# Optimization experiments

Hardware: AMD Instinct MI355X
Metric: run time of the kernel (lower is better)

Reference implementation:

```python
import jax, jax.numpy as jnp
import numpy as np

D_MODEL = 1024
N_HEADS = 16
D_HEAD = D_MODEL // N_HEADS
BATCH = 2
SEQ = 2048


def spectral_linear(x, basis, scales):
    # (x @ U) * s @ U^T ; basis is a fixed (non-learned) square matrix
    return ((x @ basis) * scales) @ basis.T


def setup_inputs() -> dict:
    key = jax.random.key(0)
    ks = jax.random.split(key, 3)
    x = jax.random.normal(ks[0], (BATCH, SEQ, D_MODEL), dtype=jnp.float32)
    # orthonormal-ish spectral basis (random Gaussian scaled keeps values sane)
    basis = jax.random.normal(ks[1], (D_MODEL, D_MODEL), dtype=jnp.float32) / np.sqrt(D_MODEL)
    route_bias = jax.random.normal(ks[2], (N_HEADS, SEQ, SEQ), dtype=jnp.float32) * 0.02
    ones = jnp.ones((D_MODEL,), dtype=jnp.float32)
    return {
        "x": x,
        "basis": basis,
        "scale_q": ones,
        "scale_k": ones,
        "scale_v": ones,
        "scale_o": ones,
        "route_bias": route_bias,
    }


def reference(x, basis, scale_q, scale_k, scale_v, scale_o, route_bias):
    bsz, seq_len, _ = x.shape

    def split_heads(t):  # [b,s,d] -> [b,h,s,dh]
        return t.reshape(bsz, seq_len, N_HEADS, D_HEAD).transpose(0, 2, 1, 3)

    q = split_heads(spectral_linear(x, basis, scale_q))
    k = split_heads(spectral_linear(x, basis, scale_k))
    v = split_heads(spectral_linear(x, basis, scale_v))

    scores = jnp.einsum("bhqd,bhkd->bhqk", q, k) / np.sqrt(D_HEAD).astype(np.float32)
    scores = scores + route_bias[None, :, :seq_len, :seq_len]
    causal = jnp.triu(jnp.ones((seq_len, seq_len), dtype=bool), k=1)
    scores = jnp.where(causal[None, None], -jnp.inf, scores)
    attn = jax.nn.softmax(scores, axis=-1)
    out = jnp.einsum("bhqk,bhkd->bhqd", attn, v)
    out = out.transpose(0, 2, 1, 3).reshape(bsz, seq_len, D_MODEL)
    return spectral_linear(out, basis, scale_o)
```

## Files before the change

### kernel.cpp

```cpp
#include <hip/hip_runtime.h>
#include <stdint.h>

#define AS1 __attribute__((address_space(1)))
#define AS3 __attribute__((address_space(3)))

typedef __bf16 bf16x8 __attribute__((ext_vector_type(8)));
typedef float f32x4 __attribute__((ext_vector_type(4)));

#if defined(__has_builtin)
#if __has_builtin(__builtin_amdgcn_global_load_lds)
#define USE_GLL 1
#else
#define USE_GLL 0
#endif
#else
#define USE_GLL 0
#endif

static __device__ __forceinline__ unsigned short f2bf(float f) {
    union { float f; uint32_t u; } v; v.f = f;
    uint32_t u = v.u + 0x7fffu + ((v.u >> 16) & 1u);
    return (unsigned short)(u >> 16);
}

__global__ void k_f32_to_bf16(const float* __restrict__ in, unsigned short* __restrict__ out, int n) {
    int idx = (blockIdx.x * 256 + threadIdx.x) * 4;
    if (idx >= n) return;
    float4 v = *(const float4*)(in + idx);
    unsigned short r[4] = { f2bf(v.x), f2bf(v.y), f2bf(v.z), f2bf(v.w) };
    *(uint2*)(out + idx) = *(const uint2*)r;
}

__global__ void k_make_scaled(const float* __restrict__ basis,
                              const float* __restrict__ sq, const float* __restrict__ sk,
                              const float* __restrict__ sv, const float* __restrict__ so,
                              unsigned short* __restrict__ Bq, unsigned short* __restrict__ Bk,
                              unsigned short* __restrict__ Bv, unsigned short* __restrict__ Bo,
                              unsigned short* __restrict__ Ub) {
    int idx = blockIdx.x * 256 + threadIdx.x;
    int k = idx & 1023;
    float b = basis[idx];
    Bq[idx] = f2bf(b * sq[k]);
    Bk[idx] = f2bf(b * sk[k]);
    Bv[idx] = f2bf(b * sv[k]);
    Bo[idx] = f2bf(b * so[k]);
    Ub[idx] = f2bf(b);
}

__global__ void k_transpose_v(const unsigned short* __restrict__ vsb, unsigned short* __restrict__ vtb) {
    __shared__ __align__(16) unsigned short t[128 * 72];
    const int sc = blockIdx.x;
    const int bh = blockIdx.y;
    const int tid = threadIdx.x;
    #pragma unroll
    for (int rep = 0; rep < 4; ++rep) {
        int idx = rep * 256 + tid;
        int s = idx >> 3, part = idx & 7;
        *(uint4*)(t + s * 72 + part * 8) =
            *(const uint4*)(vsb + ((size_t)bh * 2048 + sc * 128 + s) * 64 + part * 8);
    }
    __syncthreads();
    #pragma unroll
    for (int rep = 0; rep < 4; ++rep) {
        int idx = rep * 256 + tid;
        int d = idx >> 4, pc = idx & 15;
        unsigned short tmp[8];
        #pragma unroll
        for (int j = 0; j < 8; ++j) tmp[j] = t[(pc * 8 + j) * 72 + d];
        *(uint4*)(vtb + ((size_t)bh * 64 + d) * 2048 + sc * 128 + pc * 8) = *(const uint4*)tmp;
    }
}

#define BK 32

__global__ __launch_bounds__(256, 2)
void k_gemm_qkv(const unsigned short* __restrict__ A,
                const unsigned short* __restrict__ B,
                unsigned short* __restrict__ qkv,
                int M, int N, int K)
{
    __shared__ __align__(16) unsigned short As[128 * BK];
    __shared__ __align__(16) unsigned short Bs[128 * BK];

    const int tid  = threadIdx.x;
    const int lane = tid & 63;
    const int w    = tid >> 6;
    const int wm   = w & 1;
    const int wn   = w >> 1;
    const int bm   = blockIdx.y;
    const int bn   = blockIdx.x;
    const int fm   = lane & 15;
    const int quad = lane >> 4;
    const int fk   = quad * 8;
    const int srow = lane >> 2;
    const int spart= lane & 3;

    f32x4 zero4 = {0.f, 0.f, 0.f, 0.f};
    f32x4 acc[4][4];
    #pragma unroll
    for (int i = 0; i < 4; ++i)
        #pragma unroll
        for (int j = 0; j < 4; ++j) acc[i][j] = zero4;

    for (int k0 = 0; k0 < K; k0 += BK) {
        #pragma unroll
        for (int t = 0; t < 2; ++t) {
            int row = w * 32 + t * 16 + srow;
            const unsigned short* ga = A + (size_t)(bm * 128 + row) * K + k0 + spart * 8;
            const unsigned short* gb = B + (size_t)(bn * 128 + row) * K + k0 + spart * 8;
#if USE_GLL
            __builtin_amdgcn_global_load_lds((const void AS1*)ga, (void AS3*)(As + w * 1024 + t * 512), 16, 0, 0);
            __builtin_amdgcn_global_load_lds((const void AS1*)gb, (void AS3*)(Bs + w * 1024 + t * 512), 16, 0, 0);
#else
            *(uint4*)(As + w * 1024 + t * 512 + lane * 8) = *(const uint4*)ga;
            *(uint4*)(Bs + w * 1024 + t * 512 + lane * 8) = *(const uint4*)gb;
#endif
        }
        __syncthreads();
        bf16x8 af[4], bfr[4];
        #pragma unroll
        for (int i = 0; i < 4; ++i) af[i] = *(const bf16x8*)(As + (wm * 64 + i * 16 + fm) * BK + fk);
        #pragma unroll
        for (int j = 0; j < 4; ++j) bfr[j] = *(const bf16x8*)(Bs + (wn * 64 + j * 16 + fm) * BK + fk);
        #pragma unroll
        for (int i = 0; i < 4; ++i)
            #pragma unroll
            for (int j = 0; j < 4; ++j)
                acc[i][j] = __builtin_amdgcn_mfma_f32_16x16x32_bf16(af[i], bfr[j], acc[i][j], 0, 0, 0);
        __syncthreads();
    }

    #pragma unroll
    for (int i = 0; i < 4; ++i)
        #pragma unroll
        for (int j = 0; j < 4; ++j)
            #pragma unroll
            for (int r = 0; r < 4; ++r) {
                int row = bm * 128 + wm * 64 + i * 16 + quad * 4 + r;
                int col = bn * 128 + wn * 64 + j * 16 + fm;
                int sec = col >> 10, cc = col & 1023;
                int bb = row >> 11, s = row & 2047;
                int hh = cc >> 6,  d = cc & 63;
                qkv[((size_t)sec << 22) + (((size_t)(bb * 16 + hh)) * 2048 + s) * 64 + d] = f2bf(acc[i][j][r]);
            }
}

template<int EPI>
__global__ __launch_bounds__(256, 2)
void k_gemm_n64(const unsigned short* __restrict__ A,
                const unsigned short* __restrict__ B,
                void* __restrict__ Cout,
                int M, int N, int K)
{
    __shared__ __align__(16) unsigned short As[128 * BK];
    __shared__ __align__(16) unsigned short Bs[64 * BK];

    const int tid  = threadIdx.x;
    const int lane = tid & 63;
    const int w    = tid >> 6;
    const int wm   = w & 1;
    const int wn   = w >> 1;
    const int bm   = blockIdx.y;
    const int bn   = blockIdx.x;
    const int fm   = lane & 15;
    const int quad = lane >> 4;
    const int fk   = quad * 8;
    const int srow = lane >> 2;
    const int spart= lane & 3;

    f32x4 zero4 = {0.f, 0.f, 0.f, 0.f};
    f32x4 acc[4][2];
    #pragma unroll
    for (int i = 0; i < 4; ++i)
        #pragma unroll
        for (int j = 0; j < 2; ++j) acc[i][j] = zero4;

    for (int k0 = 0; k0 < K; k0 += BK) {
        #pragma unroll
        for (int t = 0; t < 2; ++t) {
            int row = w * 32 + t * 16 + srow;
            const unsigned short* ga = A + (size_t)(bm * 128 + row) * K + k0 + spart * 8;
#if USE_GLL
            __builtin_amdgcn_global_load_lds((const void AS1*)ga, (void AS3*)(As + w * 1024 + t * 512), 16, 0, 0);
#else
            *(uint4*)(As + w * 1024 + t * 512 + lane * 8) = *(const uint4*)ga;
#endif
        }
        {
            const unsigned short* gb = B + (size_t)(bn * 64 + w * 16 + srow) * K + k0 + spart * 8;
#if USE_GLL
            __builtin_amdgcn_global_load_lds((const void AS1*)gb, (void AS3*)(Bs + w * 512), 16, 0, 0);
#else
            *(uint4*)(Bs + w * 512 + lane * 8) = *(const uint4*)gb;
#endif
        }
        __syncthreads();
        bf16x8 af[4], bfr[2];
        #pragma unroll
        for (int i = 0; i < 4; ++i) af[i] = *(const bf16x8*)(As + (wm * 64 + i * 16 + fm) * BK + fk);
        #pragma unroll
        for (int j = 0; j < 2; ++j) bfr[j] = *(const bf16x8*)(Bs + (wn * 32 + j * 16 + fm) * BK + fk);
        #pragma unroll
        for (int i = 0; i < 4; ++i)
            #pragma unroll
            for (int j = 0; j < 2; ++j)
                acc[i][j] = __builtin_amdgcn_mfma_f32_16x16x32_bf16(af[i], bfr[j], acc[i][j], 0, 0, 0);
        __syncthreads();
    }

    #pragma unroll
    for (int i = 0; i < 4; ++i)
        #pragma unroll
        for (int j = 0; j < 2; ++j)
            #pragma unroll
            for (int r = 0; r < 4; ++r) {
                int row = bm * 128 + wm * 64 + i * 16 + quad * 4 + r;
                int col = bn * 64 + wn * 32 + j * 16 + fm;
                if (EPI == 0) ((unsigned short*)Cout)[(size_t)row * N + col] = f2bf(acc[i][j][r]);
                else          ((float*)Cout)[(size_t)row * N + col] = acc[i][j][r];
            }
}

__global__ __launch_bounds__(256, 2)
void k_attn(const unsigned short* __restrict__ qs, const unsigned short* __restrict__ ks,
            const unsigned short* __restrict__ vt, const float* __restrict__ bias,
            unsigned short* __restrict__ out)
{
    const int qt = 15 - blockIdx.x;
    const int by = blockIdx.y;
    const int h  = by >> 1;
    const int b  = by & 1;
    const int bh = b * 16 + h;
    const size_t rowbase = (size_t)bh * 2048;

    const int tid  = threadIdx.x;
    const int lane = tid & 63;
    const int w    = tid >> 6;
    const int fm   = lane & 15;
    const int quad = lane >> 4;
    const int fk   = quad * 8;

    __shared__ __align__(16) unsigned short Ks[64 * 72];
    __shared__ __align__(16) unsigned short Vt[64 * 72];
    __shared__ __align__(16) unsigned short Ps[4][32 * 72];

    const int q0 = qt * 128 + w * 32;

    bf16x8 qf[2][2];
    #pragma unroll
    for (int g = 0; g < 2; ++g)
        #pragma unroll
        for (int c = 0; c < 2; ++c)
            qf[g][c] = *(const bf16x8*)(qs + (rowbase + q0 + g * 16 + fm) * 64 + c * 32 + fk);

    f32x4 zero4 = {0.f, 0.f, 0.f, 0.f};
    f32x4 oacc[2][4];
    float lsum[2][4];
    #pragma unroll
    for (int g = 0; g < 2; ++g) {
        #pragma unroll
        for (int jd = 0; jd < 4; ++jd) oacc[g][jd] = zero4;
        #pragma unroll
        for (int r = 0; r < 4; ++r) lsum[g][r] = 0.f;
    }

    const int nkt = qt * 2 + 2;
    for (int kt = 0; kt < nkt; ++kt) {
        float bb[2][4][4];
        #pragma unroll
        for (int g = 0; g < 2; ++g)
            #pragma unroll
            for (int jn = 0; jn < 4; ++jn)
                #pragma unroll
                for (int r = 0; r < 4; ++r)
                    bb[g][jn][r] = bias[((size_t)h * 2048 + q0 + g * 16 + quad * 4 + r) * 2048
                                        + kt * 64 + jn * 16 + fm];

        #pragma unroll
        for (int rep = 0; rep < 2; ++rep) {
            int idx  = rep * 256 + tid;
            int row  = idx >> 3;
            int part = idx & 7;
            *(uint4*)(Ks + row * 72 + part * 8) =
                *(const uint4*)(ks + (rowbase + kt * 64 + row) * 64 + part * 8);
            *(uint4*)(Vt + row * 72 + part * 8) =
                *(const uint4*)(vt + ((size_t)bh * 64 + row) * 2048 + kt * 64 + part * 8);
        }
        __syncthreads();

        bf16x8 kb[4][2];
        #pragma unroll
        for (int jn = 0; jn < 4; ++jn)
            #pragma unroll
            for (int c = 0; c < 2; ++c)
                kb[jn][c] = *(const bf16x8*)(Ks + (jn * 16 + fm) * 72 + c * 32 + fk);
        f32x4 sacc[2][4];
        #pragma unroll
        for (int g = 0; g < 2; ++g)
            #pragma unroll
            for (int jn = 0; jn < 4; ++jn) sacc[g][jn] = zero4;
        #pragma unroll
        for (int g = 0; g < 2; ++g)
            #pragma unroll
            for (int jn = 0; jn < 4; ++jn)
                #pragma unroll
                for (int c = 0; c < 2; ++c)
                    sacc[g][jn] = __builtin_amdgcn_mfma_f32_16x16x32_bf16(qf[g][c], kb[jn][c], sacc[g][jn], 0, 0, 0);

        #pragma unroll
        for (int g = 0; g < 2; ++g)
            #pragma unroll
            for (int jn = 0; jn < 4; ++jn)
                #pragma unroll
                for (int r = 0; r < 4; ++r) {
                    int row = q0 + g * 16 + quad * 4 + r;
                    int col = kt * 64 + jn * 16 + fm;
                    float p = exp2f(sacc[g][jn][r] * 0.18033688f + bb[g][jn][r] * 1.44269504f);
                    p = (col > row) ? 0.f : p;
                    lsum[g][r] += p;
                    Ps[w][(g * 16 + quad * 4 + r) * 72 + jn * 16 + fm] = f2bf(p);
                }

        bf16x8 vf[4][2], pf[2][2];
        #pragma unroll
        for (int jd = 0; jd < 4; ++jd)
            #pragma unroll
            for (int c = 0; c < 2; ++c)
                vf[jd][c] = *(const bf16x8*)(Vt + (jd * 16 + fm) * 72 + c * 32 + fk);
        #pragma unroll
        for (int g = 0; g < 2; ++g)
            #pragma unroll
            for (int c = 0; c < 2; ++c)
                pf[g][c] = *(const bf16x8*)(Ps[w] + (g * 16 + fm) * 72 + c * 32 + fk);
        #pragma unroll
        for (int g = 0; g < 2; ++g)
            #pragma unroll
            for (int jd = 0; jd < 4; ++jd)
                #pragma unroll
                for (int c = 0; c < 2; ++c)
                    oacc[g][jd] = __builtin_amdgcn_mfma_f32_16x16x32_bf16(pf[g][c], vf[jd][c], oacc[g][jd], 0, 0, 0);

        __syncthreads();
    }

    #pragma unroll
    for (int g = 0; g < 2; ++g)
        #pragma unroll
        for (int r = 0; r < 4; ++r) {
            float l = lsum[g][r];
            #pragma unroll
            for (int off = 1; off < 16; off <<= 1) l += __shfl_xor(l, off, 64);
            lsum[g][r] = 1.f / l;
        }

    #pragma unroll
    for (int g = 0; g < 2; ++g)
        #pragma unroll
        for (int jd = 0; jd < 4; ++jd)
            #pragma unroll
            for (int r = 0; r < 4; ++r) {
                int row = q0 + g * 16 + quad * 4 + r;
                int d   = jd * 16 + fm;
                out[((size_t)b * 2048 + row) * 1024 + h * 64 + d] = f2bf(oacc[g][jd][r] * lsum[g][r]);
            }
}

extern "C" void kernel_launch(void* const* d_in, const int* in_sizes, int n_in,
                              void* d_out, int out_size, void* d_ws, size_t ws_size,
                              hipStream_t stream) {
    (void)in_sizes; (void)n_in; (void)out_size; (void)ws_size;
    const float* x     = (const float*)d_in[0];
    const float* basis = (const float*)d_in[1];
    const float* sq    = (const float*)d_in[2];
    const float* sk    = (const float*)d_in[3];
    const float* sv    = (const float*)d_in[4];
    const float* so    = (const float*)d_in[5];
    const float* bias  = (const float*)d_in[6];
    float* out = (float*)d_out;

    char* ws = (char*)d_ws;
    size_t off = 0;
    auto alloc = [&](size_t bytes) { void* p = ws + off; off += bytes; return p; };
    unsigned short* x_bf  = (unsigned short*)alloc((size_t)8 << 20);
    unsigned short* Acat  = (unsigned short*)alloc((size_t)8 << 20);
    unsigned short* Ub    = (unsigned short*)alloc((size_t)2 << 20);
    unsigned short* Wall  = (unsigned short*)alloc((size_t)8 << 20);
    unsigned short* qkvb  = (unsigned short*)alloc((size_t)24 << 20);
    unsigned short* vtb   = (unsigned short*)alloc((size_t)8 << 20);
    unsigned short* attno = (unsigned short*)alloc((size_t)8 << 20);

    unsigned short* Bq  = Acat;
    unsigned short* Bk  = Acat + ((size_t)1 << 20);
    unsigned short* Bv  = Acat + ((size_t)2 << 20);
    unsigned short* Bo  = Acat + ((size_t)3 << 20);
    unsigned short* qsb = qkvb;
    unsigned short* ksb = qkvb + ((size_t)1 << 22);
    unsigned short* vsb = qkvb + ((size_t)2 << 22);
    unsigned short* Wo  = Wall + (size_t)3 * 1024 * 1024;

    k_f32_to_bf16<<<4096, 256, 0, stream>>>(x, x_bf, 4096 * 1024);
    k_make_scaled<<<4096, 256, 0, stream>>>(basis, sq, sk, sv, so, Bq, Bk, Bv, Bo, Ub);

    dim3 blk(256);
    k_gemm_n64<0><<<dim3(16, 32), blk, 0, stream>>>(Acat, Ub, Wall, 4096, 1024, 1024);
    k_gemm_qkv<<<dim3(24, 32), blk, 0, stream>>>(x_bf, Wall, qkvb, 4096, 3072, 1024);
    k_transpose_v<<<dim3(16, 32), blk, 0, stream>>>(vsb, vtb);
    k_attn<<<dim3(16, 32), blk, 0, stream>>>(qsb, ksb, vtb, bias, attno);
    k_gemm_n64<2><<<dim3(16, 32), blk, 0, stream>>>(attno, Wo, out, 4096, 1024, 1024);
}
```

Measured before the change: 511.6 us.

## Rewrite QKV GEMM as 256x256 triple-buffered 8-wave kernel and merge prep kernels

The QKV projection GEMM goes from a 128x128 tile with 4 waves and single-buffered synchronous LDS staging to a 256x256 tile with 8 waves. The new kernel triple-buffers direct global-to-LDS loads, splits each k-step into two MFMA phases with interleaved loads, raises wave priority around the MFMA blocks, and remaps block IDs for L2 locality. The two preprocessing kernels (x conversion and scaled-basis build) are merged into one launch to save a kernel launch. The bigger tile cuts global traffic per FLOP but uses much more LDS and registers, and the grid shrinks to 192 blocks, which may underfill the GPU.

```diff
diff --git a/kernel.cpp b/kernel.cpp
--- a/kernel.cpp
+++ b/kernel.cpp
@@ -23,28 +23,29 @@
     return (unsigned short)(u >> 16);
 }
 
-__global__ void k_f32_to_bf16(const float* __restrict__ in, unsigned short* __restrict__ out, int n) {
-    int idx = (blockIdx.x * 256 + threadIdx.x) * 4;
-    if (idx >= n) return;
-    float4 v = *(const float4*)(in + idx);
-    unsigned short r[4] = { f2bf(v.x), f2bf(v.y), f2bf(v.z), f2bf(v.w) };
-    *(uint2*)(out + idx) = *(const uint2*)r;
-}
-
-__global__ void k_make_scaled(const float* __restrict__ basis,
-                              const float* __restrict__ sq, const float* __restrict__ sk,
-                              const float* __restrict__ sv, const float* __restrict__ so,
-                              unsigned short* __restrict__ Bq, unsigned short* __restrict__ Bk,
-                              unsigned short* __restrict__ Bv, unsigned short* __restrict__ Bo,
-                              unsigned short* __restrict__ Ub) {
-    int idx = blockIdx.x * 256 + threadIdx.x;
-    int k = idx & 1023;
-    float b = basis[idx];
-    Bq[idx] = f2bf(b * sq[k]);
-    Bk[idx] = f2bf(b * sk[k]);
-    Bv[idx] = f2bf(b * sv[k]);
-    Bo[idx] = f2bf(b * so[k]);
-    Ub[idx] = f2bf(b);
+__global__ void k_prep(const float* __restrict__ x, const float* __restrict__ basis,
+                       const float* __restrict__ sq, const float* __restrict__ sk,
+                       const float* __restrict__ sv, const float* __restrict__ so,
+                       unsigned short* __restrict__ x_bf,
+                       unsigned short* __restrict__ Bq, unsigned short* __restrict__ Bk,
+                       unsigned short* __restrict__ Bv, unsigned short* __restrict__ Bo,
+                       unsigned short* __restrict__ Ub) {
+    int b = blockIdx.x;
+    if (b < 4096) {
+        int idx = b * 256 + threadIdx.x;
+        int k = idx & 1023;
+        float v = basis[idx];
+        Bq[idx] = f2bf(v * sq[k]);
+        Bk[idx] = f2bf(v * sk[k]);
+        Bv[idx] = f2bf(v * sv[k]);
+        Bo[idx] = f2bf(v * so[k]);
+        Ub[idx] = f2bf(v);
+    } else {
+        int idx = ((b - 4096) * 256 + threadIdx.x) * 4;
+        float4 v = *(const float4*)(x + idx);
+        unsigned short r[4] = { f2bf(v.x), f2bf(v.y), f2bf(v.z), f2bf(v.w) };
+        *(uint2*)(x_bf + idx) = *(const uint2*)r;
+    }
 }
 
 __global__ void k_transpose_v(const unsigned short* __restrict__ vsb, unsigned short* __restrict__ vtb) {
@@ -71,73 +72,103 @@
     }
 }
 
-#define BK 32
-
-__global__ __launch_bounds__(256, 2)
-void k_gemm_qkv(const unsigned short* __restrict__ A,
-                const unsigned short* __restrict__ B,
-                unsigned short* __restrict__ qkv,
-                int M, int N, int K)
+__global__ __launch_bounds__(512, 2)
+void k_gemm_qkv8(const unsigned short* __restrict__ A,
+                 const unsigned short* __restrict__ B,
+                 unsigned short* __restrict__ qkv)
 {
-    __shared__ __align__(16) unsigned short As[128 * BK];
-    __shared__ __align__(16) unsigned short Bs[128 * BK];
+    __shared__ __align__(16) unsigned short lds[3 * 16384];
 
     const int tid  = threadIdx.x;
     const int lane = tid & 63;
     const int w    = tid >> 6;
     const int wm   = w & 1;
     const int wn   = w >> 1;
-    const int bm   = blockIdx.y;
-    const int bn   = blockIdx.x;
     const int fm   = lane & 15;
     const int quad = lane >> 4;
-    const int fk   = quad * 8;
-    const int srow = lane >> 2;
-    const int spart= lane & 3;
+    const int K    = 1024;
+    const int NT   = 32;
+
+    int bid  = blockIdx.y * 12 + blockIdx.x;
+    int sbid = (bid & 7) * 24 + (bid >> 3);
+    const int bm = sbid / 12;
+    const int bn = sbid % 12;
+
+    const int srow = tid >> 2;
+    const int sg   = tid & 3;
+    const unsigned short* gA = A + ((size_t)(bm * 256) + srow) * K + sg * 8;
+    const unsigned short* gB = B + ((size_t)(bn * 256) + srow) * K + sg * 8;
+
+#define STAGE_A8(tt, h) __builtin_amdgcn_global_load_lds( \
+        (const void AS1*)(gA + (size_t)(h) * 128 * 1024 + (tt) * 32), \
+        (void AS3*)(lds + ((tt) % 3) * 16384 + (h) * 4096 + w * 512), 16, 0, 0)
+#define STAGE_B8(tt, h) __builtin_amdgcn_global_load_lds( \
+        (const void AS1*)(gB + (size_t)(h) * 128 * 1024 + (tt) * 32), \
+        (void AS3*)(lds + ((tt) % 3) * 16384 + 8192 + (h) * 4096 + w * 512), 16, 0, 0)
 
     f32x4 zero4 = {0.f, 0.f, 0.f, 0.f};
-    f32x4 acc[4][4];
-    #pragma unroll
-    for (int i = 0; i < 4; ++i)
+    f32x4 acc[8][4];
+    #pragma unroll
+    for (int i = 0; i < 8; ++i)
         #pragma unroll
         for (int j = 0; j < 4; ++j) acc[i][j] = zero4;
 
-    for (int k0 = 0; k0 < K; k0 += BK) {
-        #pragma unroll
-        for (int t = 0; t < 2; ++t) {
-            int row = w * 32 + t * 16 + srow;
-            const unsigned short* ga = A + (size_t)(bm * 128 + row) * K + k0 + spart * 8;
-            const unsigned short* gb = B + (size_t)(bn * 128 + row) * K + k0 + spart * 8;
-#if USE_GLL
-            __builtin_amdgcn_global_load_lds((const void AS1*)ga, (void AS3*)(As + w * 1024 + t * 512), 16, 0, 0);
-            __builtin_amdgcn_global_load_lds((const void AS1*)gb, (void AS3*)(Bs + w * 1024 + t * 512), 16, 0, 0);
-#else
-            *(uint4*)(As + w * 1024 + t * 512 + lane * 8) = *(const uint4*)ga;
-            *(uint4*)(Bs + w * 1024 + t * 512 + lane * 8) = *(const uint4*)gb;
-#endif
-        }
-        __syncthreads();
-        bf16x8 af[4], bfr[4];
-        #pragma unroll
-        for (int i = 0; i < 4; ++i) af[i] = *(const bf16x8*)(As + (wm * 64 + i * 16 + fm) * BK + fk);
-        #pragma unroll
-        for (int j = 0; j < 4; ++j) bfr[j] = *(const bf16x8*)(Bs + (wn * 64 + j * 16 + fm) * BK + fk);
+    STAGE_A8(0, 0); STAGE_A8(0, 1); STAGE_B8(0, 0); STAGE_B8(0, 1);
+    STAGE_A8(1, 0); STAGE_A8(1, 1); STAGE_B8(1, 0); STAGE_B8(1, 1);
+    asm volatile("s_waitcnt vmcnt(4)" ::: "memory");
+    __builtin_amdgcn_s_barrier();
+
+    for (int t = 0; t < NT; ++t) {
+        const unsigned short* buf = lds + (t % 3) * 16384;
+
+        bf16x8 bfr[4], af[4];
+        #pragma unroll
+        for (int j = 0; j < 4; ++j)
+            bfr[j] = *(const bf16x8*)(buf + 8192 + (wn * 64 + j * 16 + fm) * 32 + quad * 8);
+        #pragma unroll
+        for (int i = 0; i < 4; ++i)
+            af[i] = *(const bf16x8*)(buf + (wm * 128 + i * 16 + fm) * 32 + quad * 8);
+        if (t + 2 < NT) { STAGE_A8(t + 2, 0); STAGE_A8(t + 2, 1); }
+        __builtin_amdgcn_s_barrier();
+        asm volatile("s_waitcnt lgkmcnt(0)" ::: "memory");
+        __builtin_amdgcn_s_setprio(1);
         #pragma unroll
         for (int i = 0; i < 4; ++i)
             #pragma unroll
             for (int j = 0; j < 4; ++j)
                 acc[i][j] = __builtin_amdgcn_mfma_f32_16x16x32_bf16(af[i], bfr[j], acc[i][j], 0, 0, 0);
-        __syncthreads();
-    }
-
-    #pragma unroll
-    for (int i = 0; i < 4; ++i)
+        __builtin_amdgcn_s_setprio(0);
+        __builtin_amdgcn_s_barrier();
+
+        bf16x8 af2[4];
+        #pragma unroll
+        for (int i = 0; i < 4; ++i)
+            af2[i] = *(const bf16x8*)(buf + (wm * 128 + 64 + i * 16 + fm) * 32 + quad * 8);
+        if (t + 2 < NT) { STAGE_B8(t + 2, 0); STAGE_B8(t + 2, 1); }
+        if (t < NT - 2)       asm volatile("s_waitcnt vmcnt(4)" ::: "memory");
+        else if (t == NT - 2) asm volatile("s_waitcnt vmcnt(0)" ::: "memory");
+        __builtin_amdgcn_s_barrier();
+        asm volatile("s_waitcnt lgkmcnt(0)" ::: "memory");
+        __builtin_amdgcn_s_setprio(1);
+        #pragma unroll
+        for (int i = 0; i < 4; ++i)
+            #pragma unroll
+            for (int j = 0; j < 4; ++j)
+                acc[i + 4][j] = __builtin_amdgcn_mfma_f32_16x16x32_bf16(af2[i], bfr[j], acc[i + 4][j], 0, 0, 0);
+        __builtin_amdgcn_s_setprio(0);
+        __builtin_amdgcn_s_barrier();
+    }
+#undef STAGE_A8
+#undef STAGE_B8
+
+    #pragma unroll
+    for (int i = 0; i < 8; ++i)
         #pragma unroll
         for (int j = 0; j < 4; ++j)
             #pragma unroll
             for (int r = 0; r < 4; ++r) {
-                int row = bm * 128 + wm * 64 + i * 16 + quad * 4 + r;
-                int col = bn * 128 + wn * 64 + j * 16 + fm;
+                int row = bm * 256 + wm * 128 + i * 16 + quad * 4 + r;
+                int col = bn * 256 + wn * 64 + j * 16 + fm;
                 int sec = col >> 10, cc = col & 1023;
                 int bb = row >> 11, s = row & 2047;
                 int hh = cc >> 6,  d = cc & 63;
@@ -145,6 +176,7 @@
             }
 }
 
+#define BK 32
 template<int EPI>
 __global__ __launch_bounds__(256, 2)
 void k_gemm_n64(const unsigned short* __restrict__ A,
@@ -398,12 +430,11 @@
     unsigned short* vsb = qkvb + ((size_t)2 << 22);
     unsigned short* Wo  = Wall + (size_t)3 * 1024 * 1024;
 
-    k_f32_to_bf16<<<4096, 256, 0, stream>>>(x, x_bf, 4096 * 1024);
-    k_make_scaled<<<4096, 256, 0, stream>>>(basis, sq, sk, sv, so, Bq, Bk, Bv, Bo, Ub);
+    k_prep<<<8192, 256, 0, stream>>>(x, basis, sq, sk, sv, so, x_bf, Bq, Bk, Bv, Bo, Ub);
 
     dim3 blk(256);
     k_gemm_n64<0><<<dim3(16, 32), blk, 0, stream>>>(Acat, Ub, Wall, 4096, 1024, 1024);
-    k_gemm_qkv<<<dim3(24, 32), blk, 0, stream>>>(x_bf, Wall, qkvb, 4096, 3072, 1024);
+    k_gemm_qkv8<<<dim3(12, 16), dim3(512), 0, stream>>>(x_bf, Wall, qkvb);
     k_transpose_v<<<dim3(16, 32), blk, 0, stream>>>(vsb, vtb);
     k_attn<<<dim3(16, 32), blk, 0, stream>>>(qsb, ksb, vtb, bias, attno);
     k_gemm_n64<2><<<dim3(16, 32), blk, 0, stream>>>(attno, Wo, out, 4096, 1024, 1024);
```

Measured after the change: 510.5 us. No clear change (-0.2%).
